# Optimization experiments

Hardware: AMD Instinct MI355X
Metric: run time of the kernel (lower is better)

The kernel has to match this reference:

```python
import jax, jax.numpy as jnp
import numpy as np

ALPHA = 1.5   # entmax alpha (module init arg)
N_ITER = 50   # bisection iterations (EntmaxBisect default in this repo)


def _entmax_bisect(X):
    """alpha-entmax over last dim via bisection; faithful to EntmaxBisectFunction.forward."""
    a = ALPHA
    Xs = X * (a - 1.0)
    d = Xs.shape[-1]
    max_val = jnp.max(Xs, axis=-1, keepdims=True)
    tau_lo = max_val - 1.0                      # _gp(1, alpha) == 1
    tau_hi = max_val - (1.0 / d) ** (a - 1.0)   # _gp(1/d, alpha)

    def p(tau):  # _p: clamp then ** (1/(alpha-1))
        return jnp.clip(Xs - tau, 0.0) ** (1.0 / (a - 1.0))

    f_lo = jnp.sum(p(tau_lo), axis=-1, keepdims=True) - 1.0
    dm0 = tau_hi - tau_lo

    def body(i, carry):
        tau_lo, dm, _ = carry
        dm = dm * 0.5
        tau_m = tau_lo + dm
        f_m = jnp.sum(p(tau_m), axis=-1, keepdims=True) - 1.0
        mask = (f_m * f_lo) >= 0.0
        tau_lo = jnp.where(mask, tau_m, tau_lo)
        return (tau_lo, dm, tau_m)

    _, _, tau_m = jax.lax.fori_loop(0, N_ITER, body, (tau_lo, dm0, tau_lo))
    P = p(tau_m)
    return P / jnp.sum(P, axis=-1, keepdims=True)  # ensure_sum_one


def setup_inputs() -> dict:
    key = jax.random.key(0)
    k0, k1, k2, k3 = jax.random.split(key, 4)
    B, R = 1, 4096
    NFIELD, NEMB, H = 65, 256, 8
    HD, DK = NEMB // H, NEMB
    x = jax.random.normal(k0, (B, R, NFIELD * NEMB), dtype=jnp.float32)
    # xavier-ish scales for the learned params
    bilinear_w = jax.random.normal(k1, (H, HD, DK), dtype=jnp.float32) * 0.15
    query = jax.random.normal(k2, (H, DK), dtype=jnp.float32) * 0.15
    values = jax.random.normal(k3, (H, NFIELD - 1), dtype=jnp.float32) * 0.3
    return {"x": x, "bilinear_w": bilinear_w, "query": query, "values": values}


def reference(x, bilinear_w, query, values):
    # x: [1, R, nfield*nemb]  (leading dim must be 1; torch.squeeze in source assumes it)
    B, R, D = x.shape
    h, dk = query.shape
    nemb = dk               # d_k == nemb in ExponentialNeuron
    nfield = D // nemb
    hd = nemb // h
    scale = nemb ** -0.5

    xr = x.reshape(R, nfield, nemb)                       # squeeze b=1: [R, f, e]
    # rearrange 'b r c (h hd) -> h r c hd' (b squeezed)
    keys = xr[:, 1:, :].reshape(R, nfield - 1, h, hd).transpose(2, 0, 1, 3)
    # att_gates: einsum('h r c d, h d k, h k -> h r c') * scale
    att = jnp.einsum('hrcd,hdk,hk->hrc', keys, bilinear_w, query) * scale
    gates = _entmax_bisect(att)                           # [h, R, c]
    cross_weight = gates * values[:, None, :]             # einsum('hbf,hf->hbf')
    # x_cross = exp(einsum('bfe,hbf->bhe'))
    x_cross = jnp.exp(jnp.einsum('rfe,hrf->rhe', xr[:, 1:, :], cross_weight))
    x_cross = x_cross.reshape(B, R, h * nemb)
    return jnp.concatenate([x, x_cross], axis=-1)         # [1, R, (nfield+h)*nemb]
```

## Files before the change

### kernel.cpp

```cpp
#include <hip/hip_runtime.h>
#include <math.h>

namespace {

constexpr int kRows = 4096;
constexpr int kNF   = 65;
constexpr int kNE   = 256;
constexpr int kNH   = 8;
constexpr int kNC   = 64;
constexpr int kXRow = kNF * kNE;
constexpr int kORow = (kNF + kNH) * kNE;

typedef float vf4 __attribute__((ext_vector_type(4)));

__device__ __forceinline__ void nt_store4(const float4& v, float4* dst) {
  vf4 t = {v.x, v.y, v.z, v.w};
  __builtin_nontemporal_store(t, reinterpret_cast<vf4*>(dst));
}

__global__ __launch_bounds__(256) void w2_precompute(
    const float* __restrict__ bw, const float* __restrict__ query,
    float* __restrict__ w2) {
  const int t = threadIdx.x;
  const int h = t >> 5;
  const float4* __restrict__ b4 = reinterpret_cast<const float4*>(bw) + (size_t)t * 64;
  const float4* __restrict__ q4 = reinterpret_cast<const float4*>(query) + (size_t)h * 64;
  float acc = 0.f;
#pragma unroll 8
  for (int k = 0; k < 64; ++k) {
    const float4 b = b4[k];
    const float4 q = q4[k];
    acc += b.x * q.x + b.y * q.y + b.z * q.z + b.w * q.w;
  }
  w2[t] = acc;
}

__global__ __launch_bounds__(512) void fused_row(
    const float* __restrict__ x, const float* __restrict__ w2g,
    const float* __restrict__ vals, float* __restrict__ out) {
  __shared__ float att_t[kNC * 9];
  __shared__ float cw[kNC * kNH];
  __shared__ float4 part[8 * 2 * 64];

  const int tid  = threadIdx.x;
  const int wv   = tid >> 6;
  const int lane = tid & 63;
  const int r    = blockIdx.x;

  const float* __restrict__ xrow = x + (size_t)r * kXRow;
  float* __restrict__ orow       = out + (size_t)r * kORow;
  const float4* __restrict__ x4  = reinterpret_cast<const float4*>(xrow);
  float4* __restrict__ o4        = reinterpret_cast<float4*>(orow);

  float4 kreg[8];
  const float4 wq = reinterpret_cast<const float4*>(w2g)[lane];
  float4 v0;
  if (wv == 0) v0 = x4[lane];
#pragma unroll
  for (int j = 0; j < 8; ++j) {
    kreg[j] = x4[(wv * 8 + j + 1) * 64 + lane];
  }
  if (wv == 0) nt_store4(v0, &o4[lane]);
#pragma unroll
  for (int j = 0; j < 8; ++j) {
    const int c = wv * 8 + j;
    const float4 v = kreg[j];
    nt_store4(v, &o4[(c + 1) * 64 + lane]);
    float p = v.x * wq.x + v.y * wq.y + v.z * wq.z + v.w * wq.w;
    p += __shfl_xor(p, 1);
    p += __shfl_xor(p, 2);
    p += __shfl_xor(p, 4);
    if ((lane & 7) == 0) att_t[c * 9 + (lane >> 3)] = p * 0.03125f;
  }
  __syncthreads();

  {
    const int h  = lane >> 3;
    const int kk = lane & 7;
    float X[8];
#pragma unroll
    for (int j = 0; j < 8; ++j) X[j] = att_t[(kk * 8 + j) * 9 + h];

    float mx = X[0];
#pragma unroll
    for (int j = 1; j < 8; ++j) mx = fmaxf(mx, X[j]);
    mx = fmaxf(mx, __shfl_xor(mx, 1));
    mx = fmaxf(mx, __shfl_xor(mx, 2));
    mx = fmaxf(mx, __shfl_xor(mx, 4));

    float tau_lo = mx - 1.0f;
    float dm     = 0.875f;
    float f_lo = 0.f;
#pragma unroll
    for (int j = 0; j < 8; ++j) {
      float t = fmaxf(X[j] - tau_lo, 0.f);
      f_lo += t * t;
    }
    f_lo += __shfl_xor(f_lo, 1);
    f_lo += __shfl_xor(f_lo, 2);
    f_lo += __shfl_xor(f_lo, 4);
    f_lo -= 1.0f;

    float tau_m = tau_lo;
    for (int it = 0; it < 50; ++it) {
      dm *= 0.5f;
      tau_m = tau_lo + dm;
      float fm = 0.f;
#pragma unroll
      for (int j = 0; j < 8; ++j) {
        float t = fmaxf(X[j] - tau_m, 0.f);
        fm += t * t;
      }
      fm += __shfl_xor(fm, 1);
      fm += __shfl_xor(fm, 2);
      fm += __shfl_xor(fm, 4);
      fm -= 1.0f;
      tau_lo = (fm * f_lo >= 0.f) ? tau_m : tau_lo;
      if (__all(tau_lo + dm * 0.5f == tau_lo)) {
        tau_m = tau_lo;
        break;
      }
    }

    float s = 0.f;
    float p[8];
#pragma unroll
    for (int j = 0; j < 8; ++j) {
      float t = fmaxf(X[j] - tau_m, 0.f);
      p[j] = t * t;
      s += p[j];
    }
    s += __shfl_xor(s, 1);
    s += __shfl_xor(s, 2);
    s += __shfl_xor(s, 4);
    const float inv = 1.0f / s;
    const float* __restrict__ vrow = vals + h * kNC + kk * 8;
#pragma unroll
    for (int j = 0; j < 8; ++j) {
      cw[(kk * 8 + j) * kNH + h] = p[j] * inv * vrow[j];
    }
  }

  const float2* __restrict__ cw2 = reinterpret_cast<const float2*>(cw);
  const float* partf             = reinterpret_cast<const float*>(part);
#pragma unroll
  for (int hh = 0; hh < 4; ++hh) {
    float4 a0 = make_float4(0.f, 0.f, 0.f, 0.f);
    float4 a1 = make_float4(0.f, 0.f, 0.f, 0.f);
#pragma unroll
    for (int j = 0; j < 8; ++j) {
      const float4 kv = kreg[j];
      const float2 ca = cw2[(wv * 8 + j) * 4 + hh];
      a0.x += ca.x * kv.x; a0.y += ca.x * kv.y; a0.z += ca.x * kv.z; a0.w += ca.x * kv.w;
      a1.x += ca.y * kv.x; a1.y += ca.y * kv.y; a1.z += ca.y * kv.z; a1.w += ca.y * kv.w;
    }
    part[wv * 128 + lane]      = a0;
    part[wv * 128 + 64 + lane] = a1;
    __syncthreads();
    {
      float s = partf[tid];
#pragma unroll
      for (int sl = 1; sl < 8; ++sl) s += partf[sl * 512 + tid];
      __builtin_nontemporal_store(__expf(s), &orow[kXRow + hh * 512 + tid]);
    }
    __syncthreads();
  }
}

}

extern "C" void kernel_launch(void* const* d_in, const int* in_sizes, int n_in,
                              void* d_out, int out_size, void* d_ws, size_t ws_size,
                              hipStream_t stream) {
  const float* x     = reinterpret_cast<const float*>(d_in[0]);
  const float* bw    = reinterpret_cast<const float*>(d_in[1]);
  const float* query = reinterpret_cast<const float*>(d_in[2]);
  const float* vals  = reinterpret_cast<const float*>(d_in[3]);
  float* out = reinterpret_cast<float*>(d_out);
  float* w2  = reinterpret_cast<float*>(d_ws);

  hipLaunchKernelGGL(w2_precompute, dim3(1), dim3(256), 0, stream, bw, query, w2);
  hipLaunchKernelGGL(fused_row, dim3(kRows), dim3(512), 0, stream, x, w2, vals, out);
}
```

Baseline: 120.9 us.

## Use Newton iteration for entmax threshold, widen head blocking, parallelize w2 precompute

Replaces the bisection search for the entmax threshold with a Newton-style update on tau (using sum of t and t^2), capped at 16 iterations with early exit. This cuts the serial iteration count per row. The cross-weight accumulation now processes 4 heads per pass, halving the number of reduce/sync rounds at the cost of doubling shared partial storage. The tiny w2 precompute is spread over 32 blocks with shuffle reductions. Newton may converge to a slightly different tau than the reference bisection would.

```diff
diff --git a/kernel.cpp b/kernel.cpp
--- a/kernel.cpp
+++ b/kernel.cpp
@@ -21,18 +21,24 @@
 __global__ __launch_bounds__(256) void w2_precompute(
     const float* __restrict__ bw, const float* __restrict__ query,
     float* __restrict__ w2) {
-  const int t = threadIdx.x;
+  const int o = threadIdx.x >> 5;
+  const int l = threadIdx.x & 31;
+  const int t = blockIdx.x * 8 + o;
   const int h = t >> 5;
-  const float4* __restrict__ b4 = reinterpret_cast<const float4*>(bw) + (size_t)t * 64;
-  const float4* __restrict__ q4 = reinterpret_cast<const float4*>(query) + (size_t)h * 64;
-  float acc = 0.f;
-#pragma unroll 8
-  for (int k = 0; k < 64; ++k) {
-    const float4 b = b4[k];
-    const float4 q = q4[k];
-    acc += b.x * q.x + b.y * q.y + b.z * q.z + b.w * q.w;
-  }
-  w2[t] = acc;
+  const float4* __restrict__ bp =
+      reinterpret_cast<const float4*>(bw + (size_t)t * 256 + l * 8);
+  const float4* __restrict__ qp =
+      reinterpret_cast<const float4*>(query + (size_t)h * 256 + l * 8);
+  const float4 b0 = bp[0], b1 = bp[1];
+  const float4 q0 = qp[0], q1 = qp[1];
+  float acc = b0.x * q0.x + b0.y * q0.y + b0.z * q0.z + b0.w * q0.w
+            + b1.x * q1.x + b1.y * q1.y + b1.z * q1.z + b1.w * q1.w;
+  acc += __shfl_xor(acc, 1);
+  acc += __shfl_xor(acc, 2);
+  acc += __shfl_xor(acc, 4);
+  acc += __shfl_xor(acc, 8);
+  acc += __shfl_xor(acc, 16);
+  if (l == 0) w2[t] = acc;
 }
 
 __global__ __launch_bounds__(512) void fused_row(
@@ -40,7 +46,7 @@
     const float* __restrict__ vals, float* __restrict__ out) {
   __shared__ float att_t[kNC * 9];
   __shared__ float cw[kNC * kNH];
-  __shared__ float4 part[8 * 2 * 64];
+  __shared__ float4 part[8 * 4 * 64];
 
   const int tid  = threadIdx.x;
   const int wv   = tid >> 6;
@@ -88,45 +94,29 @@
     mx = fmaxf(mx, __shfl_xor(mx, 2));
     mx = fmaxf(mx, __shfl_xor(mx, 4));
 
-    float tau_lo = mx - 1.0f;
-    float dm     = 0.875f;
-    float f_lo = 0.f;
-#pragma unroll
-    for (int j = 0; j < 8; ++j) {
-      float t = fmaxf(X[j] - tau_lo, 0.f);
-      f_lo += t * t;
-    }
-    f_lo += __shfl_xor(f_lo, 1);
-    f_lo += __shfl_xor(f_lo, 2);
-    f_lo += __shfl_xor(f_lo, 4);
-    f_lo -= 1.0f;
-
-    float tau_m = tau_lo;
-    for (int it = 0; it < 50; ++it) {
-      dm *= 0.5f;
-      tau_m = tau_lo + dm;
-      float fm = 0.f;
+    float tau = mx - 1.0f;
+    for (int it = 0; it < 16; ++it) {
+      float s2 = 0.f, s1 = 0.f;
 #pragma unroll
       for (int j = 0; j < 8; ++j) {
-        float t = fmaxf(X[j] - tau_m, 0.f);
-        fm += t * t;
+        const float t = fmaxf(X[j] - tau, 0.f);
+        s2 += t * t;
+        s1 += t;
       }
-      fm += __shfl_xor(fm, 1);
-      fm += __shfl_xor(fm, 2);
-      fm += __shfl_xor(fm, 4);
-      fm -= 1.0f;
-      tau_lo = (fm * f_lo >= 0.f) ? tau_m : tau_lo;
-      if (__all(tau_lo + dm * 0.5f == tau_lo)) {
-        tau_m = tau_lo;
-        break;
-      }
+      s2 += __shfl_xor(s2, 1); s1 += __shfl_xor(s1, 1);
+      s2 += __shfl_xor(s2, 2); s1 += __shfl_xor(s1, 2);
+      s2 += __shfl_xor(s2, 4); s1 += __shfl_xor(s1, 4);
+      const float delta = (s2 - 1.0f) / (2.0f * fmaxf(s1, 1e-30f));
+      const float ntau = tau + delta;
+      if (__all(ntau == tau)) break;
+      tau = ntau;
     }
 
     float s = 0.f;
     float p[8];
 #pragma unroll
     for (int j = 0; j < 8; ++j) {
-      float t = fmaxf(X[j] - tau_m, 0.f);
+      const float t = fmaxf(X[j] - tau, 0.f);
       p[j] = t * t;
       s += p[j];
     }
@@ -141,29 +131,37 @@
     }
   }
 
-  const float2* __restrict__ cw2 = reinterpret_cast<const float2*>(cw);
+  const float4* __restrict__ cw4 = reinterpret_cast<const float4*>(cw);
   const float* partf             = reinterpret_cast<const float*>(part);
 #pragma unroll
-  for (int hh = 0; hh < 4; ++hh) {
+  for (int hh = 0; hh < 2; ++hh) {
     float4 a0 = make_float4(0.f, 0.f, 0.f, 0.f);
     float4 a1 = make_float4(0.f, 0.f, 0.f, 0.f);
+    float4 a2 = make_float4(0.f, 0.f, 0.f, 0.f);
+    float4 a3 = make_float4(0.f, 0.f, 0.f, 0.f);
 #pragma unroll
     for (int j = 0; j < 8; ++j) {
       const float4 kv = kreg[j];
-      const float2 ca = cw2[(wv * 8 + j) * 4 + hh];
+      const float4 ca = cw4[(wv * 8 + j) * 2 + hh];
       a0.x += ca.x * kv.x; a0.y += ca.x * kv.y; a0.z += ca.x * kv.z; a0.w += ca.x * kv.w;
       a1.x += ca.y * kv.x; a1.y += ca.y * kv.y; a1.z += ca.y * kv.z; a1.w += ca.y * kv.w;
+      a2.x += ca.z * kv.x; a2.y += ca.z * kv.y; a2.z += ca.z * kv.z; a2.w += ca.z * kv.w;
+      a3.x += ca.w * kv.x; a3.y += ca.w * kv.y; a3.z += ca.w * kv.z; a3.w += ca.w * kv.w;
     }
-    part[wv * 128 + lane]      = a0;
-    part[wv * 128 + 64 + lane] = a1;
+    part[wv * 256 + 0 * 64 + lane] = a0;
+    part[wv * 256 + 1 * 64 + lane] = a1;
+    part[wv * 256 + 2 * 64 + lane] = a2;
+    part[wv * 256 + 3 * 64 + lane] = a3;
     __syncthreads();
-    {
-      float s = partf[tid];
 #pragma unroll
-      for (int sl = 1; sl < 8; ++sl) s += partf[sl * 512 + tid];
-      __builtin_nontemporal_store(__expf(s), &orow[kXRow + hh * 512 + tid]);
+    for (int oo = 0; oo < 2; ++oo) {
+      const int o = oo * 512 + tid;
+      float s = partf[o];
+#pragma unroll
+      for (int sl = 1; sl < 8; ++sl) s += partf[sl * 1024 + o];
+      __builtin_nontemporal_store(__expf(s), &orow[kXRow + hh * 1024 + o]);
     }
-    __syncthreads();
+    if (hh == 0) __syncthreads();
   }
 }
 
@@ -179,6 +177,6 @@
   float* out = reinterpret_cast<float*>(d_out);
   float* w2  = reinterpret_cast<float*>(d_ws);
 
-  hipLaunchKernelGGL(w2_precompute, dim3(1), dim3(256), 0, stream, bw, query, w2);
+  hipLaunchKernelGGL(w2_precompute, dim3(32), dim3(256), 0, stream, bw, query, w2);
   hipLaunchKernelGGL(fused_row, dim3(kRows), dim3(512), 0, stream, x, w2, vals, out);
 }
```

Result: faster. 107.6 us (-11.0%).
